# Kernel tuning notes

Hardware: AMD Instinct MI355X
Metric: run time of the kernel (lower is better)

The kernel has to match this reference:

```python
import jax, jax.numpy as jnp
import numpy as np

HIDDEN = 2560
HEADS = 32
HEAD_DIM = HIDDEN // HEADS  # 80
ROT = HEAD_DIM // 2         # partial_rotary_factor=0.5 -> 40
B = 2
S = 2048
T = B * S
THETA = 10000.0


def setup_inputs() -> dict:
    key = jax.random.key(0)
    k0, k1, k2, k3, k4 = jax.random.split(key, 5)
    hidden_states = jax.random.normal(k0, (T, HIDDEN), jnp.float32)
    w_qkv = jax.random.normal(k1, (3 * HIDDEN, HIDDEN), jnp.float32) * 0.02
    b_qkv = jax.random.normal(k2, (3 * HIDDEN,), jnp.float32) * 0.02
    w_o = jax.random.normal(k3, (HIDDEN, HIDDEN), jnp.float32) * 0.02
    b_o = jax.random.normal(k4, (HIDDEN,), jnp.float32) * 0.02
    # rotary tables for positions 0..S-1 per sequence, rotary_dim=ROT
    pos = jnp.tile(jnp.arange(S, dtype=jnp.float32), B)  # [T]
    inv_freq = 1.0 / (THETA ** (jnp.arange(0, ROT, 2, dtype=jnp.float32) / ROT))  # [ROT//2]
    freqs = pos[:, None] * inv_freq[None, :]  # [T, ROT//2]
    return {
        "hidden_states": hidden_states,
        "w_qkv": w_qkv,
        "b_qkv": b_qkv,
        "w_o": w_o,
        "b_o": b_o,
        "cos": jnp.cos(freqs),
        "sin": jnp.sin(freqs),
        "batch": B,
    }


def _apply_rope(x, cos, sin):
    # x: [T, H, D]; rotate first ROT dims NeoX-style (rotate_half)
    half = ROT // 2
    x1 = x[..., :half]
    x2 = x[..., half:ROT]
    c = cos[:, None, :]
    s = sin[:, None, :]
    return jnp.concatenate([x1 * c - x2 * s, x1 * s + x2 * c, x[..., ROT:]], axis=-1)


def reference(hidden_states, w_qkv, b_qkv, w_o, b_o, cos, sin, batch):
    t, hdim = hidden_states.shape
    seq = t // batch
    # fused QKV projection (with bias)
    qkv = hidden_states @ w_qkv.T + b_qkv  # [T, 3*HIDDEN]
    q, k, v = jnp.split(qkv, 3, axis=1)
    q = _apply_rope(q.reshape(t, HEADS, HEAD_DIM), cos, sin)
    k = _apply_rope(k.reshape(t, HEADS, HEAD_DIM), cos, sin)
    v = v.reshape(t, HEADS, HEAD_DIM)
    # prefill causal attention per sequence
    qb = q.reshape(batch, seq, HEADS, HEAD_DIM)
    kb = k.reshape(batch, seq, HEADS, HEAD_DIM)
    vb = v.reshape(batch, seq, HEADS, HEAD_DIM)
    scale = 1.0 / jnp.sqrt(jnp.float32(HEAD_DIM))
    scores = jnp.einsum("bqhd,bkhd->bhqk", qb, kb) * scale  # [B,H,S,S]
    causal = jnp.tril(jnp.ones((seq, seq), dtype=bool))
    scores = jnp.where(causal[None, None], scores, jnp.finfo(scores.dtype).min)
    attn = jax.nn.softmax(scores, axis=-1)
    out = jnp.einsum("bhqk,bkhd->bqhd", attn, vb).reshape(t, HIDDEN)
    return out @ w_o.T + b_o
```

## Files before the change

kernel.cpp:

```cpp
#include <hip/hip_runtime.h>
#include <hip/hip_bf16.h>

#define HID   2560
#define NH    32
#define HD    80
#define SEQ   2048
#define TTOT  4096
#define QKVN  7680

typedef float  f32x4  __attribute__((ext_vector_type(4)));
typedef short  short8 __attribute__((ext_vector_type(8)));
typedef __bf16 bf16x8 __attribute__((ext_vector_type(8)));
typedef __hip_bfloat16 bf16;

__device__ __forceinline__ float bf2f(bf16 h) { return __bfloat162float(h); }
__device__ __forceinline__ bf16  f2bf(float f) { return __float2bfloat16(f); }

__device__ __forceinline__ f32x4 mfma16(short8 a, short8 b, f32x4 c) {
  return __builtin_amdgcn_mfma_f32_16x16x32_bf16(
      __builtin_bit_cast(bf16x8, a), __builtin_bit_cast(bf16x8, b), c, 0, 0, 0);
}

typedef __attribute__((address_space(1))) const unsigned int as1_uint;
typedef __attribute__((address_space(3))) unsigned int       as3_uint;
__device__ __forceinline__ void gld16(const void* g, void* l) {
  __builtin_amdgcn_global_load_lds((as1_uint*)g, (as3_uint*)l, 16, 0, 0);
}

__global__ void detect_kernel(const unsigned short* __restrict__ hid, int* flag) {
  const int tid = threadIdx.x;
  const unsigned short u = hid[2 * (tid * 997)];
  const int e = (u >> 7) & 0xFF;
  const int sane = (u == 0 || (e >= 0x60 && e <= 0x8A)) ? 1 : 0;
  __shared__ int cnt;
  if (tid == 0) cnt = 0;
  __syncthreads();
  atomicAdd(&cnt, sane);
  __syncthreads();
  if (tid == 0) *flag = (cnt < 160) ? 1 : 0;
}

__global__ void convert_kernel(const void* __restrict__ src, bf16* __restrict__ dst,
                               int n8, const int* __restrict__ flag) {
  const bool isf32 = (*flag != 0);
  for (int i = blockIdx.x * 256 + threadIdx.x; i < n8; i += gridDim.x * 256) {
    if (isf32) {
      const float4* s = (const float4*)src;
      float4 a = s[2 * i], b = s[2 * i + 1];
      __align__(16) bf16 o8[8] = {f2bf(a.x), f2bf(a.y), f2bf(a.z), f2bf(a.w),
                                  f2bf(b.x), f2bf(b.y), f2bf(b.z), f2bf(b.w)};
      *(uint4*)(dst + 8 * i) = *(const uint4*)o8;
    } else {
      *(uint4*)(dst + 8 * i) = ((const uint4*)src)[i];
    }
  }
}

__global__ void emit_kernel(const bf16* __restrict__ src, void* __restrict__ dst,
                            int n8, const int* __restrict__ flag) {
  const bool isf32 = (*flag != 0);
  for (int i = blockIdx.x * 256 + threadIdx.x; i < n8; i += gridDim.x * 256) {
    uint4 v = *(const uint4*)(src + 8 * i);
    if (isf32) {
      const bf16* b = (const bf16*)&v;
      float4* d = (float4*)dst;
      d[2 * i]     = make_float4(bf2f(b[0]), bf2f(b[1]), bf2f(b[2]), bf2f(b[3]));
      d[2 * i + 1] = make_float4(bf2f(b[4]), bf2f(b[5]), bf2f(b[6]), bf2f(b[7]));
    } else {
      ((uint4*)dst)[i] = v;
    }
  }
}

__global__ __launch_bounds__(512, 2) void gemm256_bias(
    const bf16* __restrict__ A, const bf16* __restrict__ B,
    const bf16* __restrict__ bias, bf16* __restrict__ C,
    int M, int N, int K)
{
  __shared__ __align__(16) bf16 lds[2][2][16384];

  const int tid  = threadIdx.x;
  const int wid  = tid >> 6;
  const int lane = tid & 63;
  const int quad = lane >> 4;
  const int l15  = lane & 15;
  const int wr   = wid >> 2;
  const int wc   = wid & 3;

  int wgid;
  {
    const int nwg = gridDim.x;
    const int q = nwg >> 3, r = nwg & 7;
    const int xcd = blockIdx.x & 7, lin = blockIdx.x >> 3;
    wgid = (xcd < r ? xcd * (q + 1) : r * (q + 1) + (xcd - r) * q) + lin;
  }
  const int gx = M >> 8;
  const int m0 = (wgid % gx) << 8;
  const int n0 = (wgid / gx) << 8;

  const int NT = K >> 6;

  const int rr   = tid >> 3;
  const int cbyt = ((tid & 7) << 4) ^ ((rr & 7) << 4);
  const size_t o1 = (size_t)rr * K + (cbyt >> 1);
  const size_t o2 = o1 + (size_t)64 * K;

  const bf16* Ab = A + (size_t)m0 * K;
  const bf16* Bb = B + (size_t)n0 * K;

#define STAGE(which, bufsel, half, tt)                                         \
  {                                                                            \
    const bf16* _s = ((which) ? Bb : Ab) + (size_t)(half) * 128 * K + (tt) * 64;\
    bf16* _d = &lds[bufsel][which][(half) * 8192 + wid * 512];                 \
    gld16(_s + o1, _d);                                                        \
    gld16(_s + o2, _d + 4096);                                                 \
  }

  const int csw0 = ((quad ^ (l15 & 7)) << 4);
  const int csw1 = (((4 | quad) ^ (l15 & 7)) << 4);

  f32x4 acc[8][4];
#pragma unroll
  for (int i = 0; i < 8; ++i)
#pragma unroll
    for (int j = 0; j < 4; ++j) acc[i][j] = (f32x4)0.f;

  short8 a[4][2], b[4][2];

  STAGE(0, 0, 0, 0); STAGE(0, 0, 1, 0);
  STAGE(1, 0, 0, 0); STAGE(1, 0, 1, 0);
  STAGE(1, 1, 0, 1); STAGE(1, 1, 1, 1);
  asm volatile("s_waitcnt vmcnt(4)" ::: "memory");
  __builtin_amdgcn_s_barrier();

  for (int t = 0; t < NT; ++t) {
    const int cur = t & 1, nxt = cur ^ 1;
    const bf16* Al = lds[cur][0];
    const bf16* Bl = lds[cur][1];

#pragma unroll
    for (int mi = 0; mi < 4; ++mi) {
      const char* p = (const char*)Al + (size_t)(wr * 128 + mi * 16 + l15) * 128;
      a[mi][0] = *(const short8*)(p + csw0);
      a[mi][1] = *(const short8*)(p + csw1);
    }
#pragma unroll
    for (int n = 0; n < 2; ++n) {
      const char* p = (const char*)Bl + (size_t)(wc * 64 + n * 16 + l15) * 128;
      b[n][0] = *(const short8*)(p + csw0);
      b[n][1] = *(const short8*)(p + csw1);
    }
    if (t + 1 < NT) STAGE(0, nxt, 0, t + 1);
    __builtin_amdgcn_s_barrier();
    asm volatile("s_waitcnt lgkmcnt(0)" ::: "memory");
    __builtin_amdgcn_sched_barrier(0);
    __builtin_amdgcn_s_setprio(1);
#pragma unroll
    for (int mi = 0; mi < 4; ++mi)
#pragma unroll
      for (int n = 0; n < 2; ++n) {
        acc[mi][n] = mfma16(a[mi][0], b[n][0], acc[mi][n]);
        acc[mi][n] = mfma16(a[mi][1], b[n][1], acc[mi][n]);
      }
    __builtin_amdgcn_s_setprio(0);
    __builtin_amdgcn_s_barrier();

#pragma unroll
    for (int n = 2; n < 4; ++n) {
      const char* p = (const char*)Bl + (size_t)(wc * 64 + n * 16 + l15) * 128;
      b[n][0] = *(const short8*)(p + csw0);
      b[n][1] = *(const short8*)(p + csw1);
    }
    if (t + 1 < NT) STAGE(0, nxt, 1, t + 1);
    __builtin_amdgcn_s_barrier();
    asm volatile("s_waitcnt lgkmcnt(0)" ::: "memory");
    __builtin_amdgcn_sched_barrier(0);
    __builtin_amdgcn_s_setprio(1);
#pragma unroll
    for (int mi = 0; mi < 4; ++mi)
#pragma unroll
      for (int n = 2; n < 4; ++n) {
        acc[mi][n] = mfma16(a[mi][0], b[n][0], acc[mi][n]);
        acc[mi][n] = mfma16(a[mi][1], b[n][1], acc[mi][n]);
      }
    __builtin_amdgcn_s_setprio(0);
    __builtin_amdgcn_s_barrier();

#pragma unroll
    for (int mi = 0; mi < 4; ++mi) {
      const char* p = (const char*)Al + (size_t)(wr * 128 + 64 + mi * 16 + l15) * 128;
      a[mi][0] = *(const short8*)(p + csw0);
      a[mi][1] = *(const short8*)(p + csw1);
    }
    if (t + 2 < NT) STAGE(1, cur, 0, t + 2);
    __builtin_amdgcn_s_barrier();
    asm volatile("s_waitcnt lgkmcnt(0)" ::: "memory");
    __builtin_amdgcn_sched_barrier(0);
    __builtin_amdgcn_s_setprio(1);
#pragma unroll
    for (int mi = 0; mi < 4; ++mi)
#pragma unroll
      for (int n = 2; n < 4; ++n) {
        acc[4 + mi][n] = mfma16(a[mi][0], b[n][0], acc[4 + mi][n]);
        acc[4 + mi][n] = mfma16(a[mi][1], b[n][1], acc[4 + mi][n]);
      }
    __builtin_amdgcn_s_setprio(0);
    __builtin_amdgcn_s_barrier();

    if (t + 2 < NT) STAGE(1, cur, 1, t + 2);
    __builtin_amdgcn_s_barrier();
    __builtin_amdgcn_s_setprio(1);
#pragma unroll
    for (int mi = 0; mi < 4; ++mi)
#pragma unroll
      for (int n = 0; n < 2; ++n) {
        acc[4 + mi][n] = mfma16(a[mi][0], b[n][0], acc[4 + mi][n]);
        acc[4 + mi][n] = mfma16(a[mi][1], b[n][1], acc[4 + mi][n]);
      }
    __builtin_amdgcn_s_setprio(0);
    if (t + 2 < NT) {
      asm volatile("s_waitcnt vmcnt(4)" ::: "memory");
    } else if (t + 1 < NT) {
      asm volatile("s_waitcnt vmcnt(0)" ::: "memory");
    }
    __builtin_amdgcn_s_barrier();
  }
#undef STAGE

  const int crow = m0 + wr * 128 + quad * 4;
  const int ccol = n0 + wc * 64 + l15;
#pragma unroll
  for (int n = 0; n < 4; ++n) {
    const float bv = bf2f(bias[ccol + n * 16]);
#pragma unroll
    for (int mi = 0; mi < 8; ++mi) {
      const int rb = crow + mi * 16;
#pragma unroll
      for (int r = 0; r < 4; ++r)
        C[(size_t)(rb + r) * N + ccol + n * 16] = f2bf(acc[mi][n][r] + bv);
    }
  }
}

__global__ __launch_bounds__(256) void rope_kernel(
    const bf16* __restrict__ qkv, const bf16* __restrict__ cosb,
    const bf16* __restrict__ sinb, bf16* __restrict__ Qr, bf16* __restrict__ Kr)
{
  const int t = blockIdx.x;
  const int b = t >> 11;
  const int s = t & 2047;
  const float qscale = 0.11180339887498949f;

  __shared__ float cs[20], sn[20];
  if (threadIdx.x < 20) cs[threadIdx.x] = bf2f(cosb[t * 20 + threadIdx.x]);
  if (threadIdx.x >= 32 && threadIdx.x < 52)
    sn[threadIdx.x - 32] = bf2f(sinb[t * 20 + (threadIdx.x - 32)]);
  __syncthreads();

  const bf16* qrow = qkv + (size_t)t * QKVN;
  const bf16* krow = qrow + HID;

  for (int idx = threadIdx.x; idx < HID; idx += 256) {
    const int h = idx / HD, d = idx % HD;
    const size_t off = ((size_t)(b * NH + h) * SEQ + s) * HD + d;
    float q, k;
    if (d < 20) {
      q = bf2f(qrow[h * HD + d]) * cs[d] - bf2f(qrow[h * HD + d + 20]) * sn[d];
      k = bf2f(krow[h * HD + d]) * cs[d] - bf2f(krow[h * HD + d + 20]) * sn[d];
    } else if (d < 40) {
      q = bf2f(qrow[h * HD + d - 20]) * sn[d - 20] + bf2f(qrow[h * HD + d]) * cs[d - 20];
      k = bf2f(krow[h * HD + d - 20]) * sn[d - 20] + bf2f(krow[h * HD + d]) * cs[d - 20];
    } else {
      q = bf2f(qrow[h * HD + d]);
      k = bf2f(krow[h * HD + d]);
    }
    Qr[off] = f2bf(q * qscale);
    Kr[off] = f2bf(k);
  }
}

__global__ __launch_bounds__(256) void vtrans_kernel(
    const bf16* __restrict__ qkv, bf16* __restrict__ Vt)
{
  const int bh = blockIdx.x;
  const int s0 = blockIdx.y * 64;
  const int b = bh >> 5, h = bh & 31;
  __shared__ bf16 tile[64][81];

  for (int e = threadIdx.x; e < 64 * HD; e += 256) {
    const int r = e / HD, d = e % HD;
    tile[r][d] = qkv[(size_t)(b * SEQ + s0 + r) * QKVN + 2 * HID + h * HD + d];
  }
  __syncthreads();
  for (int e = threadIdx.x; e < 64 * HD; e += 256) {
    const int d = e >> 6, r = e & 63;
    Vt[((size_t)bh * HD + d) * SEQ + s0 + r] = tile[r][d];
  }
}

__global__ __launch_bounds__(256, 3) void attn_kernel(
    const bf16* __restrict__ Qr, const bf16* __restrict__ Kr,
    const bf16* __restrict__ Vt, bf16* __restrict__ O)
{
  const int raw  = blockIdx.x;
  const int slot = raw >> 3;
  const int qblk = 15 - (slot & 15);
  const int bh   = ((slot >> 4) << 3) + (raw & 7);

  const int tid  = threadIdx.x;
  const int wave = tid >> 6;
  const int lane = tid & 63;
  const int quad = lane >> 4;
  const int l15  = lane & 15;
  const int qbase = qblk * 128;

  __shared__ __align__(16) bf16 stage[12544];
  __shared__ __align__(16) bf16 pt[4 * 2 * 1152];

  bf16* kt = stage;
  bf16* vt = stage + 5632;

  if (tid < 144) {
    const unsigned one2 = 0x3F803F80u;
    *(uint4*)&vt[5760 + tid * 8] = (uint4){one2, one2, one2, one2};
  }

  int goff[6];
#pragma unroll
  for (int it = 0; it < 6; it++) {
    const int j = tid + it * 256;
    if (j < 704) {
      const int r = j / 11; int c = j - 11 * r; if (c > 9) c = 0;
      goff[it] = r * 160 + c * 16;
    } else {
      const int j2 = j - 704;
      const int r = j2 / 9; int c = j2 - 9 * r; if (c > 7) c = 0;
      goff[it] = r * 4096 + c * 16;
    }
  }

  short8 aq[2][3];
#pragma unroll
  for (int f = 0; f < 2; f++) {
    const bf16* Qb = Qr + ((size_t)bh * SEQ + qbase + f * 64 + wave * 16 + l15) * HD + quad * 8;
    aq[f][0] = *(const short8*)(Qb);
    aq[f][1] = *(const short8*)(Qb + 32);
    aq[f][2] = *(const short8*)(Qb + 64);
    if (quad >= 2) aq[f][2] = (short8)0;
  }

  f32x4 o[2][6];
#pragma unroll
  for (int f = 0; f < 2; f++)
    for (int nt = 0; nt < 6; nt++) o[f][nt] = (f32x4)0.f;
  float m_i[2] = {-3e38f, -3e38f};

  const char* Kb8 = (const char*)(Kr + (size_t)bh * SEQ * HD);
  const char* Vb8 = (const char*)(Vt + (size_t)bh * HD * SEQ);
  const int nsteps = 2 * qblk + 2;
  const int rmax0 = qbase + wave * 16 + 15;

  for (int step = 0; step < nsteps; step++) {
    const int kvo = step * 64;
    const bool act0 = (kvo <= rmax0);

    __syncthreads();
    {
      const char* kb = Kb8 + kvo * 160;
      const char* vb = Vb8 + kvo * 2;
#pragma unroll
      for (int it = 0; it < 6; it++) {
        const int j = tid + it * 256;
        if (j < 1424) {
          bf16* ldsb = stage + (it * 256 + wave * 64) * 8;
          gld16((j < 704) ? (kb + goff[it]) : (vb + goff[it]), ldsb);
        }
      }
    }
    __syncthreads();

    f32x4 sv[2][4];
#pragma unroll
    for (int nt = 0; nt < 4; nt++) {
      const bf16* kr = &kt[(nt * 16 + l15) * 88 + quad * 8];
      short8 b0 = *(const short8*)(kr);
      short8 b1 = *(const short8*)(kr + 32);
      short8 b2 = *(const short8*)(kr + 64);
      if (act0) {
        f32x4 s = mfma16(b0, aq[0][0], (f32x4)0.f);
        s = mfma16(b1, aq[0][1], s);
        sv[0][nt] = mfma16(b2, aq[0][2], s);
      }
      f32x4 s1 = mfma16(b0, aq[1][0], (f32x4)0.f);
      s1 = mfma16(b1, aq[1][1], s1);
      sv[1][nt] = mfma16(b2, aq[1][2], s1);
    }

#pragma unroll
    for (int f = 0; f < 2; f++) {
      if (f == 0 && !act0) continue;
      const int mrel = qbase + f * 64 + wave * 16 - kvo;
      if (mrel < 63) {
        const int qrel = mrel + l15;
#pragma unroll
        for (int nt = 0; nt < 4; nt++) {
          f32x4 t = sv[f][nt];
#pragma unroll
          for (int r = 0; r < 4; r++)
            t[r] = (nt * 16 + quad * 4 + r <= qrel) ? t[r] : -3e38f;
          sv[f][nt] = t;
        }
      }
      float mx = fmaxf(fmaxf(sv[f][0][0], sv[f][0][1]), fmaxf(sv[f][0][2], sv[f][0][3]));
#pragma unroll
      for (int nt = 1; nt < 4; nt++)
        mx = fmaxf(mx, fmaxf(fmaxf(sv[f][nt][0], sv[f][nt][1]),
                             fmaxf(sv[f][nt][2], sv[f][nt][3])));
      mx = fmaxf(mx, __shfl_xor(mx, 16, 64));
      mx = fmaxf(mx, __shfl_xor(mx, 32, 64));
      const float mnew = fmaxf(m_i[f], mx);
      const float alpha = __expf(m_i[f] - mnew);
      m_i[f] = mnew;

      bf16* ptw = pt + (wave * 2 + f) * 1152;
#pragma unroll
      for (int nt = 0; nt < 4; nt++) {
        __align__(8) bf16 p4[4];
#pragma unroll
        for (int r = 0; r < 4; r++) p4[r] = f2bf(__expf(sv[f][nt][r] - mnew));
        *(unsigned long long*)&ptw[l15 * 72 + nt * 16 + quad * 4] =
            *(const unsigned long long*)p4;
      }
      float av[4];
#pragma unroll
      for (int r = 0; r < 4; r++) av[r] = __shfl(alpha, quad * 4 + r, 64);
#pragma unroll
      for (int nt = 0; nt < 6; nt++) {
        f32x4 t = o[f][nt];
        t[0] *= av[0]; t[1] *= av[1]; t[2] *= av[2]; t[3] *= av[3];
        o[f][nt] = t;
      }
    }

    asm volatile("s_waitcnt lgkmcnt(0)" ::: "memory");
    short8 pa00 = (short8)0, pa01 = (short8)0, pa10, pa11;
    {
      const bf16* p0 = pt + (wave * 2 + 0) * 1152 + l15 * 72 + quad * 8;
      const bf16* p1 = pt + (wave * 2 + 1) * 1152 + l15 * 72 + quad * 8;
      if (act0) { pa00 = *(const short8*)p0; pa01 = *(const short8*)(p0 + 32); }
      pa10 = *(const short8*)p1; pa11 = *(const short8*)(p1 + 32);
    }
#pragma unroll
    for (int nt = 0; nt < 6; nt++) {
      const bf16* vr = &vt[(nt * 16 + l15) * 72 + quad * 8];
      short8 v0 = *(const short8*)(vr);
      short8 v1 = *(const short8*)(vr + 32);
      if (act0) {
        o[0][nt] = mfma16(pa00, v0, o[0][nt]);
        o[0][nt] = mfma16(pa01, v1, o[0][nt]);
      }
      o[1][nt] = mfma16(pa10, v0, o[1][nt]);
      o[1][nt] = mfma16(pa11, v1, o[1][nt]);
    }
  }

  const int b = bh >> 5, h = bh & 31;
#pragma unroll
  for (int f = 0; f < 2; f++)
#pragma unroll
    for (int r = 0; r < 4; r++) {
      const float inv = 1.0f / o[f][5][r];
      const int trow = b * SEQ + qbase + f * 64 + wave * 16 + quad * 4 + r;
#pragma unroll
      for (int nt = 0; nt < 5; nt++)
        O[(size_t)trow * HID + h * HD + nt * 16 + l15] = f2bf(o[f][nt][r] * inv);
    }
}

extern "C" void kernel_launch(void* const* d_in, const int* in_sizes, int n_in,
                              void* d_out, int out_size, void* d_ws, size_t ws_size,
                              hipStream_t stream) {
  (void)in_sizes; (void)n_in; (void)ws_size;
  char* wsb = (char*)d_ws;

  int*  flag   = (int*) (wsb + 0);
  bf16* cos_c  = (bf16*)(wsb + 1024);
  bf16* sin_c  = (bf16*)(wsb + 165888);
  bf16* bqkv_c = (bf16*)(wsb + 329728);
  bf16* bo_c   = (bf16*)(wsb + 345088);
  bf16* wo_c   = (bf16*)(wsb + 1048576);
  bf16* qkv    = (bf16*)(wsb + 14155776);
  bf16* hid_c  = (bf16*)(wsb + 77070336);
  bf16* wqkv_c = (bf16*)(wsb + 98041856);
  bf16* Qr     = (bf16*)(wsb + 77070336);
  bf16* Kr     = (bf16*)(wsb + 98041856);
  bf16* Vt     = (bf16*)(wsb + 119013376);
  bf16* attn   = (bf16*)(wsb + 14155776);
  bf16* obuf   = (bf16*)(wsb + 35127296);

  detect_kernel<<<1, 256, 0, stream>>>((const unsigned short*)d_in[0], flag);
  convert_kernel<<<1024, 256, 0, stream>>>(d_in[0], hid_c,  TTOT * HID / 8, flag);
  convert_kernel<<<1024, 256, 0, stream>>>(d_in[1], wqkv_c, QKVN * HID / 8, flag);
  convert_kernel<<<4,    256, 0, stream>>>(d_in[2], bqkv_c, QKVN / 8,       flag);
  convert_kernel<<<1024, 256, 0, stream>>>(d_in[3], wo_c,   HID * HID / 8,  flag);
  convert_kernel<<<2,    256, 0, stream>>>(d_in[4], bo_c,   HID / 8,        flag);
  convert_kernel<<<40,   256, 0, stream>>>(d_in[5], cos_c,  TTOT * 20 / 8,  flag);
  convert_kernel<<<40,   256, 0, stream>>>(d_in[6], sin_c,  TTOT * 20 / 8,  flag);

  gemm256_bias<<<dim3((TTOT / 256) * (QKVN / 256)), 512, 0, stream>>>(
      hid_c, wqkv_c, bqkv_c, qkv, TTOT, QKVN, HID);
  rope_kernel<<<dim3(TTOT), 256, 0, stream>>>(qkv, cos_c, sin_c, Qr, Kr);
  vtrans_kernel<<<dim3(64, SEQ / 64), 256, 0, stream>>>(qkv, Vt);
  attn_kernel<<<dim3(1024), 256, 0, stream>>>(Qr, Kr, Vt, attn);
  gemm256_bias<<<dim3((TTOT / 256) * (HID / 256)), 512, 0, stream>>>(
      attn, wo_c, bo_c, obuf, TTOT, HID, HID);
  emit_kernel<<<1024, 256, 0, stream>>>(obuf, d_out, out_size / 8, flag);
}
```

Before: 600.8 us.

## Triple-buffer A tiles in GEMM to prefetch two K-steps ahead

Splits the shared LDS tile buffer into a three-deep ring for A and a two-deep ring for B. Both operands are now prefetched two K-iterations ahead instead of A only one ahead, and the vmcnt waits are adjusted to match. The aim is more latency hiding on the global-to-LDS loads. The cost is LDS growing from 128KB to 160KB per block, which likely caps occupancy below the two blocks per CU requested by launch bounds.

Result: no change. 605.9 us (+0.8%).

```diff
diff --git a/kernel.cpp b/kernel.cpp
--- a/kernel.cpp
+++ b/kernel.cpp
@@ -77,7 +77,8 @@
     const bf16* __restrict__ bias, bf16* __restrict__ C,
     int M, int N, int K)
 {
-  __shared__ __align__(16) bf16 lds[2][2][16384];
+  __shared__ __align__(16) bf16 lA[3][16384];
+  __shared__ __align__(16) bf16 lB[2][16384];
 
   const int tid  = threadIdx.x;
   const int wid  = tid >> 6;
@@ -108,13 +109,20 @@
   const bf16* Ab = A + (size_t)m0 * K;
   const bf16* Bb = B + (size_t)n0 * K;
 
-#define STAGE(which, bufsel, half, tt)                                         \
+#define STAGEA(bufsel, half, tt)                                               \
   {                                                                            \
-    const bf16* _s = ((which) ? Bb : Ab) + (size_t)(half) * 128 * K + (tt) * 64;\
-    bf16* _d = &lds[bufsel][which][(half) * 8192 + wid * 512];                 \
+    const bf16* _s = Ab + (size_t)(half) * 128 * K + (tt) * 64;                \
+    bf16* _d = &lA[bufsel][(half) * 8192 + wid * 512];                         \
     gld16(_s + o1, _d);                                                        \
     gld16(_s + o2, _d + 4096);                                                 \
   }
+#define STAGEB(bufsel, half, tt)                                               \
+  {                                                                            \
+    const bf16* _s = Bb + (size_t)(half) * 128 * K + (tt) * 64;                \
+    bf16* _d = &lB[bufsel][(half) * 8192 + wid * 512];                         \
+    gld16(_s + o1, _d);                                                        \
+    gld16(_s + o2, _d + 4096);                                                 \
+  }
 
   const int csw0 = ((quad ^ (l15 & 7)) << 4);
   const int csw1 = (((4 | quad) ^ (l15 & 7)) << 4);
@@ -127,16 +135,20 @@
 
   short8 a[4][2], b[4][2];
 
-  STAGE(0, 0, 0, 0); STAGE(0, 0, 1, 0);
-  STAGE(1, 0, 0, 0); STAGE(1, 0, 1, 0);
-  STAGE(1, 1, 0, 1); STAGE(1, 1, 1, 1);
-  asm volatile("s_waitcnt vmcnt(4)" ::: "memory");
+  STAGEA(0, 0, 0); STAGEA(0, 1, 0);
+  STAGEB(0, 0, 0); STAGEB(0, 1, 0);
+  STAGEA(1, 0, 1); STAGEA(1, 1, 1);
+  STAGEB(1, 0, 1); STAGEB(1, 1, 1);
+  asm volatile("s_waitcnt vmcnt(8)" ::: "memory");
   __builtin_amdgcn_s_barrier();
 
   for (int t = 0; t < NT; ++t) {
-    const int cur = t & 1, nxt = cur ^ 1;
-    const bf16* Al = lds[cur][0];
-    const bf16* Bl = lds[cur][1];
+    const int ac  = t % 3;
+    const int an2 = (t + 2) % 3;
+    const int bc  = t & 1;
+    const bf16* Al = lA[ac];
+    const bf16* Bl = lB[bc];
+    const bool pf = (t + 2 < NT);
 
 #pragma unroll
     for (int mi = 0; mi < 4; ++mi) {
@@ -150,7 +162,7 @@
       b[n][0] = *(const short8*)(p + csw0);
       b[n][1] = *(const short8*)(p + csw1);
     }
-    if (t + 1 < NT) STAGE(0, nxt, 0, t + 1);
+    if (pf) STAGEA(an2, 0, t + 2);
     __builtin_amdgcn_s_barrier();
     asm volatile("s_waitcnt lgkmcnt(0)" ::: "memory");
     __builtin_amdgcn_sched_barrier(0);
@@ -171,7 +183,7 @@
       b[n][0] = *(const short8*)(p + csw0);
       b[n][1] = *(const short8*)(p + csw1);
     }
-    if (t + 1 < NT) STAGE(0, nxt, 1, t + 1);
+    if (pf) STAGEA(an2, 1, t + 2);
     __builtin_amdgcn_s_barrier();
     asm volatile("s_waitcnt lgkmcnt(0)" ::: "memory");
     __builtin_amdgcn_sched_barrier(0);
@@ -192,7 +204,7 @@
       a[mi][0] = *(const short8*)(p + csw0);
       a[mi][1] = *(const short8*)(p + csw1);
     }
-    if (t + 2 < NT) STAGE(1, cur, 0, t + 2);
+    if (pf) STAGEB(bc, 0, t + 2);
     __builtin_amdgcn_s_barrier();
     asm volatile("s_waitcnt lgkmcnt(0)" ::: "memory");
     __builtin_amdgcn_sched_barrier(0);
@@ -207,7 +219,7 @@
     __builtin_amdgcn_s_setprio(0);
     __builtin_amdgcn_s_barrier();
 
-    if (t + 2 < NT) STAGE(1, cur, 1, t + 2);
+    if (pf) STAGEB(bc, 1, t + 2);
     __builtin_amdgcn_s_barrier();
     __builtin_amdgcn_s_setprio(1);
 #pragma unroll
@@ -218,14 +230,15 @@
         acc[4 + mi][n] = mfma16(a[mi][1], b[n][1], acc[4 + mi][n]);
       }
     __builtin_amdgcn_s_setprio(0);
-    if (t + 2 < NT) {
-      asm volatile("s_waitcnt vmcnt(4)" ::: "memory");
+    if (pf) {
+      asm volatile("s_waitcnt vmcnt(8)" ::: "memory");
     } else if (t + 1 < NT) {
       asm volatile("s_waitcnt vmcnt(0)" ::: "memory");
     }
     __builtin_amdgcn_s_barrier();
   }
-#undef STAGE
+#undef STAGEA
+#undef STAGEB
 
   const int crow = m0 + wr * 128 + quad * 4;
   const int ccol = n0 + wc * 64 + l15;
```
